# Performance work log

Hardware: AMD Instinct MI355X
Metric: run time of the kernel (lower is better)

Reference implementation:

```python
import jax, jax.numpy as jnp
import numpy as np

EPS = 1e-6
T = 10.0
STEPS = 3
BN_EPS = 1e-5

def _normalize(x, axis):
    n = jnp.sqrt(jnp.sum(x * x, axis=axis, keepdims=True))
    return x / jnp.maximum(n, EPS)

def _vq_step(X, D):
    # X: (B, d, n), D: (B, d, r)
    Dn = _normalize(D, 1)
    Xn = _normalize(X, 1)
    cos = jnp.einsum('bdr,bdn->brn', Dn, Xn)          # (B, r, n)
    C = jax.nn.softmax(cos / T, axis=1)               # softmax over r
    XCt = jnp.einsum('bdn,brn->bdr', X, C)            # (B, d, r)
    sums = jnp.maximum(jnp.sum(C, axis=2), EPS)       # (B, r)
    D2 = _normalize(XCt / sums[:, None, :], 1)
    Xbar = jnp.einsum('bdr,brn->bdn', D2, C)
    return D2, C, Xbar

def _ham_vq(X, D0):
    # K-1 steps without gradient tracking, final step with grad through X only
    Xs = jax.lax.stop_gradient(X)
    def body(D, _):
        D, _, _ = _vq_step(Xs, D)
        return D, None
    D, _ = jax.lax.scan(body, _normalize(D0, 1), None, length=STEPS - 1)
    D = jax.lax.stop_gradient(D)
    _, _, Xbar = _vq_step(X, D)
    return Xbar

def _conv1x1(x, w, b=None):
    y = jnp.einsum('oc,bchw->bohw', w, x)
    if b is not None:
        y = y + b[None, :, None, None]
    return y

def _bn(x, gamma, beta, mean, var):
    inv = gamma / jnp.sqrt(var + BN_EPS)
    return x * inv[None, :, None, None] + (beta - mean * inv)[None, :, None, None]


def setup_inputs() -> dict:
    key = jax.random.key(0)
    ks = jax.random.split(key, 16)
    B, Cin, H, W = 8, 512, 64, 64
    d_mid, r = 512, 64
    out_ch = 2 * d_mid  # dual
    sc = 0.02
    inp = {
        'z': jax.random.normal(ks[0], (B, Cin, H, W), jnp.float32),
        'lower_w': jax.random.normal(ks[1], (out_ch, Cin), jnp.float32) * sc,
        'lower_b': jnp.zeros((out_ch,), jnp.float32),
        'Dinit_s': jax.random.uniform(ks[2], (B, d_mid, r), jnp.float32),
        'Dinit_c': jax.random.uniform(ks[3], (B, d_mid, r), jnp.float32),
        'cheese_w': jax.random.normal(ks[4], (out_ch, out_ch), jnp.float32) * sc,
        'ch_gamma': jnp.ones((out_ch,), jnp.float32),
        'ch_beta': jnp.zeros((out_ch,), jnp.float32),
        'ch_mean': jax.random.normal(ks[5], (out_ch,), jnp.float32) * 0.1,
        'ch_var': jax.random.uniform(ks[6], (out_ch,), jnp.float32) + 0.5,
        'upper_w': jax.random.normal(ks[7], (Cin, out_ch), jnp.float32) * sc,
        'upper_b': jnp.zeros((Cin,), jnp.float32),
        'h_gamma': jnp.ones((Cin,), jnp.float32),
        'h_beta': jnp.zeros((Cin,), jnp.float32),
        'h_mean': jax.random.normal(ks[8], (Cin,), jnp.float32) * 0.1,
        'h_var': jax.random.uniform(ks[9], (Cin,), jnp.float32) + 0.5,
        'coef_ham': jnp.array(1.0, jnp.float32),
        'coef_shortcut': jnp.array(1.0, jnp.float32),
    }
    return inp


def reference(z, lower_w, lower_b, Dinit_s, Dinit_c, cheese_w,
              ch_gamma, ch_beta, ch_mean, ch_var, upper_w, upper_b,
              h_gamma, h_beta, h_mean, h_var, coef_ham, coef_shortcut):
    B, Cin, H, W = z.shape
    identity = z
    # lower: conv1x1 + relu
    y = jax.nn.relu(_conv1x1(z, lower_w, lower_b))       # (B, 2*d_mid, H, W)
    d_mid = y.shape[1] // 2
    y1, y2 = y[:, :d_mid], y[:, d_mid:]
    n = H * W
    # spatial ham
    Xs = y1.reshape(B, d_mid, n)
    y1 = _ham_vq(Xs, Dinit_s).reshape(B, d_mid, H, W)
    # channel ham (same (B, d, n) flattening; HamMD requires dim1 == d_mid)
    Xc = y2.reshape(B, d_mid, n)
    y2 = _ham_vq(Xc, Dinit_c).reshape(B, d_mid, H, W)
    y = jnp.concatenate([y1, y2], axis=1)
    # cheese: conv1x1(no bias) + BN + relu
    y = jax.nn.relu(_bn(_conv1x1(y, cheese_w), ch_gamma, ch_beta, ch_mean, ch_var))
    # upper conv1x1 + BN
    h = _bn(_conv1x1(y, upper_w, upper_b), h_gamma, h_beta, h_mean, h_var)
    out = coef_ham * h + coef_shortcut * identity
    return jax.nn.relu(out)
```

## Files before the change

kernel.cpp:

```cpp
#include <hip/hip_runtime.h>
#include <hip/hip_bf16.h>

typedef __bf16 bf16_t;
typedef __bf16 bf16x4 __attribute__((ext_vector_type(4)));
typedef __bf16 bf16x8 __attribute__((ext_vector_type(8)));
typedef float  f32x4  __attribute__((ext_vector_type(4)));

#define HEPS 1e-6f

__device__ __forceinline__ void gload16(const bf16_t* g, bf16_t* l) {
    __builtin_amdgcn_global_load_lds(
        (const __attribute__((address_space(1))) unsigned int*)(g),
        (__attribute__((address_space(3))) unsigned int*)(l),
        16, 0, 0);
}


__global__ void cvt_all_k(const float* __restrict__ wl, bf16_t* __restrict__ dwl,
                          const float* __restrict__ wc, bf16_t* __restrict__ dwc,
                          const float* __restrict__ wu, bf16_t* __restrict__ dwu) {
    int i = blockIdx.x * 256 + threadIdx.x;
    if (i < 524288) dwl[i] = (bf16_t)wl[i];
    else if (i < 1572864) { int k = i - 524288; dwc[k] = (bf16_t)wc[k]; }
    else { int k = i - 1572864; dwu[k] = (bf16_t)wu[k]; }
}

__global__ void prep_k(const float* __restrict__ chg, const float* __restrict__ chb,
                       const float* __restrict__ chm, const float* __restrict__ chv,
                       const float* __restrict__ hg, const float* __restrict__ hb,
                       const float* __restrict__ hm, const float* __restrict__ hv,
                       const float* __restrict__ ub, const float* __restrict__ cham,
                       float* __restrict__ chA, float* __restrict__ chB,
                       float* __restrict__ hA2, float* __restrict__ hB2) {
    int i = blockIdx.x * 256 + threadIdx.x;
    if (i < 1024) {
        float inv = chg[i] * rsqrtf(chv[i] + 1e-5f);
        chA[i] = inv;
        chB[i] = chb[i] - chm[i] * inv;
    }
    if (i < 512) {
        float inv = hg[i] * rsqrtf(hv[i] + 1e-5f);
        float cA = cham[0];
        hA2[i] = cA * inv;
        hB2[i] = cA * (fmaf(ub[i], inv, hb[i]) - hm[i] * inv);
    }
}

__global__ void tz_k(const float* __restrict__ z, bf16_t* __restrict__ Zt,
                     bf16_t* __restrict__ zb) {
    __shared__ bf16_t t[64][68];
    int b = blockIdx.z, kt = blockIdx.y, nt = blockIdx.x;
    const size_t boff = ((size_t)b * 512 + kt * 64) * 4096 + nt * 64;
    const float* src = z + boff;
    bf16_t* zbo = zb + boff;
    int tid = threadIdx.x;
    int kr = tid >> 4;
    int nc = (tid & 15) * 4;
    #pragma unroll
    for (int it = 0; it < 4; ++it) {
        int k = kr + it * 16;
        float4 v = *(const float4*)&src[(size_t)k * 4096 + nc];
        bf16x4 o;
        o[0] = (bf16_t)v.x; o[1] = (bf16_t)v.y; o[2] = (bf16_t)v.z; o[3] = (bf16_t)v.w;
        t[nc + 0][k] = o[0]; t[nc + 1][k] = o[1];
        t[nc + 2][k] = o[2]; t[nc + 3][k] = o[3];
        *(bf16x4*)&zbo[(size_t)k * 4096 + nc] = o;
    }
    __syncthreads();
    bf16_t* dst = Zt + ((size_t)b * 4096 + nt * 64) * 512 + kt * 64;
    int nr = tid >> 4;
    int kc = (tid & 15) * 4;
    #pragma unroll
    for (int it = 0; it < 4; ++it) {
        int n = nr + it * 16;
        bf16x4 o;
        #pragma unroll
        for (int c = 0; c < 4; ++c) o[c] = t[n][kc + c];
        *(bf16x4*)&dst[(size_t)n * 512 + kc] = o;
    }
}

__global__ void dinit_k(const float* __restrict__ Ds, const float* __restrict__ Dc,
                        bf16_t* __restrict__ Dt) {
    int bs = blockIdx.y;
    int b = bs >> 1;
    const float* src = ((bs & 1) ? Dc : Ds) + (size_t)b * 512 * 64;
    int idx = blockIdx.x * 256 + threadIdx.x;
    int r = idx & 63, d = idx >> 6;
    Dt[(size_t)bs * 64 * 512 + (size_t)r * 512 + d] = (bf16_t)src[d * 64 + r];
}

__global__ void dnorm_k(const bf16_t* __restrict__ Dt, float* __restrict__ dinv) {
    int gw = (blockIdx.x * 256 + threadIdx.x) >> 6;
    int lane = threadIdx.x & 63;
    bf16x8 v = *(const bf16x8*)(Dt + (size_t)gw * 512 + lane * 8);
    float s = 0.f;
    #pragma unroll
    for (int e = 0; e < 8; ++e) { float f = (float)v[e]; s += f * f; }
    #pragma unroll
    for (int off = 32; off > 0; off >>= 1) s += __shfl_xor(s, off);
    if (lane == 0) dinv[gw] = 1.0f / fmaxf(sqrtf(s), HEPS);
}

__global__ void reduce_k(const float* __restrict__ P, bf16_t* __restrict__ Dt,
                         float* __restrict__ dinv) {
    int bsr = blockIdx.x;
    int bs = bsr >> 6, r = bsr & 63;
    int lane = threadIdx.x;
    const float* base = P + ((size_t)(bs * 8) * 64 + r) * 512 + lane * 8;
    float s[8] = {0.f, 0.f, 0.f, 0.f, 0.f, 0.f, 0.f, 0.f};
    #pragma unroll
    for (int kc = 0; kc < 8; ++kc) {
        const float* p = base + (size_t)kc * 64 * 512;
        float4 u = *(const float4*)p;
        float4 w = *(const float4*)(p + 4);
        s[0] += u.x; s[1] += u.y; s[2] += u.z; s[3] += u.w;
        s[4] += w.x; s[5] += w.y; s[6] += w.z; s[7] += w.w;
    }
    bf16x8 o;
    float sq = 0.f;
    #pragma unroll
    for (int e = 0; e < 8; ++e) { sq += s[e] * s[e]; o[e] = (bf16_t)s[e]; }
    *(bf16x8*)&Dt[(size_t)bsr * 512 + lane * 8] = o;
    #pragma unroll
    for (int off = 32; off > 0; off >>= 1) sq += __shfl_xor(sq, off);
    if (lane == 0) dinv[bsr] = 1.0f / fmaxf(sqrtf(sq), HEPS);
}

template<int BM, int BN, int WAVES_M, int WAVES_N, int EPI, int ORDER>
__launch_bounds__(256)
__global__ void g2(const bf16_t* __restrict__ Ag, const bf16_t* __restrict__ Bg,
                   void* __restrict__ Cg, void* __restrict__ C2g,
                   const int M, const int N, const int K,
                   const int ldA, const int ldB, const int ldC,
                   const long aStride, const long bStride,
                   const long cStride, const long c2Stride,
                   const float* __restrict__ p0, const float* __restrict__ p1,
                   const float* __restrict__ scal,
                   const void* __restrict__ shortcut, const long sStride)
{
    constexpr int WM = BM / WAVES_M, WN = BN / WAVES_N;
    constexpr int FM = WM / 16, FN = WN / 16;
    constexpr int ASEG = BM / 64, BSEG = BN / 64;
    constexpr int LPT = ASEG + BSEG;

    __shared__ __align__(64) bf16_t SH[3 * (BM + BN) * 32];
    __shared__ float dl[64];
    bf16_t* Al = SH;
    bf16_t* Bl = SH + 3 * BM * 32;

    const int tid = threadIdx.x;
    const int wave = tid >> 6, lane = tid & 63;
    const int l15 = lane & 15, q = lane >> 4;
    const int lrow = lane >> 2, lcol = (lane & 3) * 8;

    const int gx = gridDim.x, gy = gridDim.y;
    const int per = gx * gy;
    const int nwg = per * gridDim.z;
    const int g = blockIdx.z * per + blockIdx.y * gx + blockIdx.x;
    const int qq = nwg >> 3, rr = nwg & 7;
    const int xcd = g & 7, jj = g >> 3;
    const int w = (xcd < rr ? xcd * (qq + 1) : rr * (qq + 1) + (xcd - rr) * qq) + jj;
    const int bz = w / per;
    const int rem = w - bz * per;
    int bx, by;
    if constexpr (ORDER == 0) { by = rem / gx; bx = rem - by * gx; }
    else                      { bx = rem / gy; by = rem - bx * gy; }

    int bs = bz, exA = 0, exB = 0;
    if constexpr (EPI == 5) { bs = bz >> 3; exA = exB = (bz & 7) * 512; }
    if constexpr (EPI == 7) { exA = (bz & 1) * 512; }

    const int n0 = bx * BN;
    const int m0 = by * BM;
    const int wm0 = (wave / WAVES_N) * WM;
    const int wn0 = (wave % WAVES_N) * WN;

    const bf16_t* Ab;
    const bf16_t* Bb;
    if constexpr (EPI == 6) {
        Ab = Ag + (size_t)(bz >> 1) * (size_t)aStride + (size_t)(bz & 1) * 512;
        Bb = Bg + (size_t)bz * (size_t)bStride;
    } else {
        Ab = Ag + (size_t)bs * (size_t)aStride + exA;
        Bb = Bg + (size_t)bs * (size_t)bStride + exB;
    }

    if constexpr (EPI == 6) { if (tid < 64) dl[tid] = p0[bz * 64 + tid]; }

    auto stage = [&](int buf, int k0) {
        #pragma unroll
        for (int t = 0; t < ASEG; ++t) {
            int seg = wave * ASEG + t;
            gload16(Ab + (size_t)(m0 + seg * 16 + lrow) * ldA + k0 + lcol,
                    &Al[buf * BM * 32 + seg * 512]);
        }
        #pragma unroll
        for (int t = 0; t < BSEG; ++t) {
            int seg = wave * BSEG + t;
            gload16(Bb + (size_t)(n0 + seg * 16 + lrow) * ldB + k0 + lcol,
                    &Bl[buf * BN * 32 + seg * 512]);
        }
    };

    f32x4 acc[FM][FN];
    #pragma unroll
    for (int i = 0; i < FM; ++i)
        #pragma unroll
        for (int j = 0; j < FN; ++j)
            #pragma unroll
            for (int e = 0; e < 4; ++e) acc[i][j][e] = 0.f;

    float xsq[FM];
    #pragma unroll
    for (int i = 0; i < FM; ++i) xsq[i] = 0.f;

    const int nK = K / 32;
    stage(0, 0);
    if (nK > 1) stage(1, 32);

    for (int t = 0; t < nK; ++t) {
        const int cur = t % 3;

        if (t < nK - 1) asm volatile("s_waitcnt vmcnt(%0)" :: "i"(LPT) : "memory");
        else            asm volatile("s_waitcnt vmcnt(0)" ::: "memory");
        asm volatile("s_barrier" ::: "memory");
        __builtin_amdgcn_sched_barrier(0);

        if (t + 2 < nK) stage((t + 2) % 3, (t + 2) * 32);

        bf16x8 af[FM], bfm[FN];
        #pragma unroll
        for (int i = 0; i < FM; ++i)
            af[i] = *(const bf16x8*)&Al[cur * BM * 32 + (wm0 + 16 * i + l15) * 32 + 8 * q];
        #pragma unroll
        for (int j = 0; j < FN; ++j)
            bfm[j] = *(const bf16x8*)&Bl[cur * BN * 32 + (wn0 + 16 * j + l15) * 32 + 8 * q];

        if constexpr (EPI == 6) {
            #pragma unroll
            for (int i = 0; i < FM; ++i)
                #pragma unroll
                for (int e = 0; e < 8; ++e) {
                    float f = (float)af[i][e];
                    xsq[i] = fmaf(f, f, xsq[i]);
                }
        }

        __builtin_amdgcn_s_setprio(1);
        #pragma unroll
        for (int i = 0; i < FM; ++i)
            #pragma unroll
            for (int j = 0; j < FN; ++j)
                acc[i][j] = __builtin_amdgcn_mfma_f32_16x16x32_bf16(af[i], bfm[j], acc[i][j], 0, 0, 0);
        __builtin_amdgcn_s_setprio(0);
    }

    int rowB[FM];
    #pragma unroll
    for (int i = 0; i < FM; ++i) rowB[i] = m0 + wm0 + 16 * i + 4 * q;
    const int colBase = n0 + wn0;

    if constexpr (EPI == 2) {
        bf16_t* O = (bf16_t*)Cg + (size_t)bz * (size_t)cStride;
        #pragma unroll
        for (int j = 0; j < FN; ++j) {
            int col = colBase + 16 * j + l15;
            float a = p0[col], b = p1[col];
            #pragma unroll
            for (int i = 0; i < FM; ++i) {
                int rb = rowB[i];
                #pragma unroll
                for (int e = 0; e < 4; ++e) {
                    float v = fmaxf(fmaf(acc[i][j][e], a, b), 0.f);
                    O[(size_t)(rb + e) * ldC + col] = (bf16_t)v;
                }
            }
        }
    } else if constexpr (EPI == 3) {
        float* O = (float*)Cg + (size_t)bz * (size_t)cStride;
        const bf16_t* scg = (const bf16_t*)shortcut + (size_t)bz * (size_t)sStride;
        bf16_t* SP = SH;
        float cB = scal[0];
        __syncthreads();
        {
            int row = tid >> 1, h = tid & 1;
            #pragma unroll
            for (int u = 0; u < 8; ++u)
                *(bf16x8*)&SP[row * 132 + h * 64 + u * 8] =
                    *(const bf16x8*)&scg[(size_t)(m0 + row) * ldC + n0 + h * 64 + u * 8];
        }
        __syncthreads();
        #pragma unroll
        for (int i = 0; i < FM; ++i) {
            int rl = wm0 + 16 * i + 4 * q;
            #pragma unroll
            for (int e = 0; e < 4; ++e) {
                int row = m0 + rl + e;
                float a = p0[row], b = p1[row];
                #pragma unroll
                for (int j = 0; j < FN; ++j) {
                    int cl = wn0 + 16 * j + l15;
                    float v = fmaf(acc[i][j][e], a, b)
                            + cB * (float)SP[(rl + e) * 132 + cl];
                    O[(size_t)row * ldC + n0 + cl] = fmaxf(v, 0.f);
                }
            }
        }
    } else if constexpr (EPI == 5) {
        float* O = (float*)Cg + (size_t)bz * (size_t)cStride;
        #pragma unroll
        for (int i = 0; i < FM; ++i) {
            int rb = rowB[i];
            #pragma unroll
            for (int j = 0; j < FN; ++j) {
                int col = colBase + 16 * j + l15;
                *(f32x4*)&O[(size_t)col * ldC + rb] = acc[i][j];
            }
        }
    } else if constexpr (EPI == 6) {
        bf16_t* Cc = (bf16_t*)Cg  + (size_t)bz * (size_t)cStride;
        bf16_t* Ct = (bf16_t*)C2g + (size_t)(bz >> 1) * (size_t)c2Stride;
        const int hoff = (bz & 1) * 64;
        const bool doCt = (C2g != nullptr);
        float xs[FM];
        #pragma unroll
        for (int i = 0; i < FM; ++i) {
            float s2 = xsq[i];
            s2 += __shfl_xor(s2, 16);
            s2 += __shfl_xor(s2, 32);
            xs[i] = s2;
        }
        float di[FN];
        #pragma unroll
        for (int j = 0; j < FN; ++j) di[j] = dl[16 * j + l15];
        #pragma unroll
        for (int i = 0; i < FM; ++i) {
            int rb = rowB[i];
            bf16x4 tj[FN];
            #pragma unroll
            for (int e = 0; e < 4; ++e) {
                float s2row = __shfl(xs[i], 4 * q + e);
                float xi = 1.0f / (10.0f * fmaxf(sqrtf(s2row), HEPS));
                float v[FN];
                float mx = -1e30f;
                #pragma unroll
                for (int j = 0; j < FN; ++j) {
                    v[j] = acc[i][j][e] * di[j] * xi;
                    mx = fmaxf(mx, v[j]);
                }
                mx = fmaxf(mx, __shfl_xor(mx, 1));
                mx = fmaxf(mx, __shfl_xor(mx, 2));
                mx = fmaxf(mx, __shfl_xor(mx, 4));
                mx = fmaxf(mx, __shfl_xor(mx, 8));
                float sm = 0.f;
                #pragma unroll
                for (int j = 0; j < FN; ++j) { v[j] = __expf(v[j] - mx); sm += v[j]; }
                sm += __shfl_xor(sm, 1);
                sm += __shfl_xor(sm, 2);
                sm += __shfl_xor(sm, 4);
                sm += __shfl_xor(sm, 8);
                float rs = 1.0f / sm;
                #pragma unroll
                for (int j = 0; j < FN; ++j) {
                    float p = v[j] * rs;
                    tj[j][e] = (bf16_t)p;
                    if (doCt) Ct[(size_t)(rb + e) * 128 + hoff + 16 * j + l15] = (bf16_t)p;
                }
            }
            #pragma unroll
            for (int j = 0; j < FN; ++j)
                *(bf16x4*)&Cc[(size_t)(16 * j + l15) * ldC + rb] = tj[j];
        }
    } else if constexpr (EPI == 7) {
        bf16_t* O = (bf16_t*)Cg + (size_t)(bz >> 1) * (size_t)cStride;
        const int hoff = (bz & 1) * 64;
        #pragma unroll
        for (int j = 0; j < FN; ++j) {
            int col = colBase + 16 * j + l15;
            float di = p0[bz * 64 + col];
            #pragma unroll
            for (int i = 0; i < FM; ++i) {
                int rb = rowB[i];
                #pragma unroll
                for (int e = 0; e < 4; ++e)
                    O[(size_t)(rb + e) * 128 + hoff + col] = (bf16_t)(acc[i][j][e] * di);
            }
        }
    } else if constexpr (EPI == 8) {
        bf16_t* O  = (bf16_t*)Cg  + (size_t)bz * (size_t)cStride;
        bf16_t* O2 = (bf16_t*)C2g + (size_t)bz * (size_t)c2Stride;
        bf16_t* SP = SH;
        __syncthreads();
        #pragma unroll
        for (int j = 0; j < FN; ++j) {
            int cl = wn0 + 16 * j + l15;
            float bias = p0[n0 + cl];
            #pragma unroll
            for (int i = 0; i < FM; ++i) {
                int rl = wm0 + 16 * i + 4 * q;
                #pragma unroll
                for (int e = 0; e < 4; ++e) {
                    float v = fmaxf(acc[i][j][e] + bias, 0.f);
                    bf16_t b = (bf16_t)v;
                    O[(size_t)(m0 + rl + e) * ldC + n0 + cl] = b;
                    SP[cl * 132 + rl + e] = b;
                }
            }
        }
        __syncthreads();
        {
            int dorow = tid >> 1, h = tid & 1;
            #pragma unroll
            for (int u = 0; u < 8; ++u) {
                bf16x8 v = *(const bf16x8*)&SP[dorow * 132 + h * 64 + u * 8];
                *(bf16x8*)&O2[(size_t)(n0 + dorow) * 4096 + m0 + h * 64 + u * 8] = v;
            }
        }
    }
}


extern "C" void kernel_launch(void* const* d_in, const int* in_sizes, int n_in,
                              void* d_out, int out_size, void* d_ws, size_t ws_size,
                              hipStream_t stream) {
    const float* z        = (const float*)d_in[0];
    const float* lower_w  = (const float*)d_in[1];
    const float* lower_b  = (const float*)d_in[2];
    const float* Dinit_s  = (const float*)d_in[3];
    const float* Dinit_c  = (const float*)d_in[4];
    const float* cheese_w = (const float*)d_in[5];
    const float* ch_gamma = (const float*)d_in[6];
    const float* ch_beta  = (const float*)d_in[7];
    const float* ch_mean  = (const float*)d_in[8];
    const float* ch_var   = (const float*)d_in[9];
    const float* upper_w  = (const float*)d_in[10];
    const float* upper_b  = (const float*)d_in[11];
    const float* h_gamma  = (const float*)d_in[12];
    const float* h_beta   = (const float*)d_in[13];
    const float* h_mean   = (const float*)d_in[14];
    const float* h_var    = (const float*)d_in[15];
    const float* coef_ham = (const float*)d_in[16];
    const float* coef_sc  = (const float*)d_in[17];

    char* ws = (char*)d_ws;
    size_t off = 0;
    auto alloc = [&](size_t bytes) -> void* {
        void* p = ws + off;
        off += (bytes + 255) & ~(size_t)255;
        return p;
    };

    bf16_t* Wl   = (bf16_t*)alloc((size_t)1024 * 512 * 2);
    bf16_t* Wc   = (bf16_t*)alloc((size_t)1024 * 1024 * 2);
    bf16_t* Wu   = (bf16_t*)alloc((size_t)512 * 1024 * 2);
    float*  chA  = (float*) alloc(1024 * 4);
    float*  chB  = (float*) alloc(1024 * 4);
    float*  hA2  = (float*) alloc(512 * 4);
    float*  hB2  = (float*) alloc(512 * 4);
    float*  dinv = (float*) alloc(1024 * 4);
    bf16_t* Xbf  = (bf16_t*)alloc((size_t)8 * 1024 * 4096 * 2);
    bf16_t* Xt   = (bf16_t*)alloc((size_t)8 * 4096 * 1024 * 2);
    bf16_t* Zt   = (bf16_t*)alloc((size_t)8 * 4096 * 512 * 2);
    bf16_t* zb   = (bf16_t*)alloc((size_t)8 * 512 * 4096 * 2);
    bf16_t* Cb   = (bf16_t*)alloc((size_t)16 * 64 * 4096 * 2);
    bf16_t* Ct2  = (bf16_t*)alloc((size_t)8 * 4096 * 128 * 2);
    float*  P    = (float*) alloc((size_t)128 * 64 * 512 * 4);
    bf16_t* Dta  = (bf16_t*)alloc((size_t)16 * 64 * 512 * 2);
    bf16_t* Dtb  = (bf16_t*)alloc((size_t)16 * 64 * 512 * 2);
    bf16_t* Eb   = (bf16_t*)alloc((size_t)8 * 1024 * 128 * 2);
    bf16_t* Ycht = Xbf;

    dim3 blk(256);

    cvt_all_k<<<8192, blk, 0, stream>>>(lower_w, Wl, cheese_w, Wc, upper_w, Wu);
    prep_k<<<4, blk, 0, stream>>>(ch_gamma, ch_beta, ch_mean, ch_var,
                                  h_gamma, h_beta, h_mean, h_var,
                                  upper_b, coef_ham, chA, chB, hA2, hB2);
    tz_k<<<dim3(64, 8, 8), blk, 0, stream>>>(z, Zt, zb);
    dinit_k<<<dim3(128, 16), blk, 0, stream>>>(Dinit_s, Dinit_c, Dta);

    g2<128, 128, 2, 2, 8, 0><<<dim3(8, 32, 8), blk, 0, stream>>>(
        Zt, Wl, (void*)Xt, (void*)Xbf, 4096, 1024, 512,
        512, 512, 1024,
        (long)4096 * 512, 0L, (long)4096 * 1024, (long)1024 * 4096,
        lower_b, nullptr, nullptr, nullptr, 0L);

    dnorm_k<<<256, blk, 0, stream>>>(Dta, dinv);

    bf16_t* cur = Dta;
    bf16_t* nxt = Dtb;
    for (int t = 0; t < 3; ++t) {
        g2<128, 64, 4, 1, 6, 0><<<dim3(1, 32, 16), blk, 0, stream>>>(
            Xt, cur, (void*)Cb, (t == 2) ? (void*)Ct2 : nullptr, 4096, 64, 512,
            1024, 512, 4096,
            (long)4096 * 1024, (long)64 * 512, (long)64 * 4096, (long)4096 * 128,
            dinv, nullptr, nullptr, nullptr, 0L);
        g2<64, 64, 2, 2, 5, 0><<<dim3(1, 8, 128), blk, 0, stream>>>(
            Xbf, Cb, (void*)P, nullptr, 512, 64, 512,
            4096, 4096, 512,
            (long)512 * 4096, (long)64 * 4096, (long)64 * 512, 0L,
            nullptr, nullptr, nullptr, nullptr, 0L);
        reduce_k<<<1024, dim3(64), 0, stream>>>(P, nxt, dinv);
        bf16_t* tmp = cur; cur = nxt; nxt = tmp;
    }

    g2<128, 64, 2, 2, 7, 0><<<dim3(1, 8, 16), blk, 0, stream>>>(
        Wc, cur, (void*)Eb, nullptr, 1024, 64, 512,
        1024, 512, 128,
        0L, (long)64 * 512, (long)1024 * 128, 0L,
        dinv, nullptr, nullptr, nullptr, 0L);

    g2<128, 128, 2, 2, 2, 0><<<dim3(8, 32, 8), blk, 0, stream>>>(
        Ct2, Eb, (void*)Ycht, nullptr, 4096, 1024, 128,
        128, 128, 1024,
        (long)4096 * 128, (long)1024 * 128, (long)4096 * 1024, 0L,
        chA, chB, nullptr, nullptr, 0L);

    g2<128, 128, 2, 2, 3, 1><<<dim3(32, 4, 8), blk, 0, stream>>>(
        Wu, Ycht, d_out, nullptr, 512, 4096, 1024,
        1024, 1024, 4096,
        0L, (long)4096 * 1024, (long)512 * 4096, 0L,
        hA2, hB2, coef_sc, zb, (long)512 * 4096);

    (void)in_sizes; (void)n_in; (void)out_size; (void)ws_size;
}
```

Measured before the change: 314.6 us.

## Drop channel-major X copy; compute X·Cᵀ from Xt with in-LDS transpose

```diff
diff --git a/kernel.cpp b/kernel.cpp
--- a/kernel.cpp
+++ b/kernel.cpp
@@ -102,29 +102,114 @@
     if (lane == 0) dinv[gw] = 1.0f / fmaxf(sqrtf(s), HEPS);
 }
 
-__global__ void reduce_k(const float* __restrict__ P, bf16_t* __restrict__ Dt,
-                         float* __restrict__ dinv) {
-    int bsr = blockIdx.x;
-    int bs = bsr >> 6, r = bsr & 63;
-    int lane = threadIdx.x;
-    const float* base = P + ((size_t)(bs * 8) * 64 + r) * 512 + lane * 8;
-    float s[8] = {0.f, 0.f, 0.f, 0.f, 0.f, 0.f, 0.f, 0.f};
-    #pragma unroll
-    for (int kc = 0; kc < 8; ++kc) {
-        const float* p = base + (size_t)kc * 64 * 512;
-        float4 u = *(const float4*)p;
-        float4 w = *(const float4*)(p + 4);
-        s[0] += u.x; s[1] += u.y; s[2] += u.z; s[3] += u.w;
-        s[4] += w.x; s[5] += w.y; s[6] += w.z; s[7] += w.w;
-    }
-    bf16x8 o;
-    float sq = 0.f;
-    #pragma unroll
-    for (int e = 0; e < 8; ++e) { sq += s[e] * s[e]; o[e] = (bf16_t)s[e]; }
-    *(bf16x8*)&Dt[(size_t)bsr * 512 + lane * 8] = o;
-    #pragma unroll
-    for (int off = 32; off > 0; off >>= 1) sq += __shfl_xor(sq, off);
-    if (lane == 0) dinv[bsr] = 1.0f / fmaxf(sqrtf(sq), HEPS);
+__global__ void reduce_k(const float* __restrict__ P, bf16_t* __restrict__ Dt) {
+    int bs = blockIdx.y;
+    int d = blockIdx.x * 4 + (threadIdx.x >> 6);
+    int r = threadIdx.x & 63;
+    float s = 0.f;
+    #pragma unroll
+    for (int kc = 0; kc < 8; ++kc)
+        s += P[(((size_t)(bs * 8 + kc)) * 512 + d) * 64 + r];
+    Dt[((size_t)bs * 64 + r) * 512 + d] = (bf16_t)s;
+}
+
+__launch_bounds__(256)
+__global__ void xct_k(const bf16_t* __restrict__ Cb, const bf16_t* __restrict__ Xt,
+                      float* __restrict__ P) {
+    __shared__ __align__(64) bf16_t Al[3][64 * 32];
+    __shared__ __align__(64) bf16_t Bl[3][64 * 40];
+
+    const int tid = threadIdx.x;
+    const int wave = tid >> 6, lane = tid & 63;
+    const int l15 = lane & 15, q = lane >> 4;
+    const int lrow = lane >> 2, lcol = (lane & 3) * 8;
+
+    const int bz = blockIdx.z;
+    const int bs = bz >> 3, kc = bz & 7;
+    const int b = bs >> 1, s = bs & 1;
+    const int d0 = blockIdx.x * 64;
+
+    const bf16_t* Ab = Cb + (size_t)bs * 64 * 4096 + kc * 512;
+    const bf16_t* Bsrc = Xt + ((size_t)b * 4096 + kc * 512) * 1024 + s * 512 + d0;
+
+    const int bn = tid >> 3;
+    const int dbase = (tid & 7) * 8;
+    const int nswz = bn ^ (((dbase >> 3) & 3) << 3);
+
+    const int wm0 = (wave >> 1) * 32;
+    const int wn0 = (wave & 1) * 32;
+
+    bf16x8 regs[2];
+
+    auto issueB = [&](int t) -> bf16x8 {
+        return *(const bf16x8*)&Bsrc[(size_t)(t * 32 + bn) * 1024 + dbase];
+    };
+    auto issueA = [&](int buf, int t) {
+        gload16(Ab + (size_t)(wave * 16 + lrow) * 4096 + t * 32 + lcol,
+                &Al[buf][wave * 512]);
+    };
+    auto writeB = [&](int buf, bf16x8 v) {
+        #pragma unroll
+        for (int e = 0; e < 8; ++e)
+            Bl[buf][(dbase + e) * 40 + nswz] = v[e];
+    };
+
+    f32x4 acc[2][2];
+    #pragma unroll
+    for (int i = 0; i < 2; ++i)
+        #pragma unroll
+        for (int j = 0; j < 2; ++j)
+            #pragma unroll
+            for (int e = 0; e < 4; ++e) acc[i][j][e] = 0.f;
+
+    const int nK = 16;
+    regs[0] = issueB(0); issueA(0, 0);
+    regs[1] = issueB(1); issueA(1, 1);
+    writeB(0, regs[0]);
+
+    for (int t = 0; t < nK; ++t) {
+        const int cur = t % 3;
+
+        if (t + 1 < nK) asm volatile("s_waitcnt vmcnt(2) lgkmcnt(0)" ::: "memory");
+        else            asm volatile("s_waitcnt vmcnt(0) lgkmcnt(0)" ::: "memory");
+        asm volatile("s_barrier" ::: "memory");
+        __builtin_amdgcn_sched_barrier(0);
+
+        if (t + 2 < nK) {
+            regs[t & 1] = issueB(t + 2);
+            issueA((t + 2) % 3, t + 2);
+        }
+        if (t + 1 < nK) writeB((t + 1) % 3, regs[(t + 1) & 1]);
+
+        bf16x8 af[2], bfm[2];
+        #pragma unroll
+        for (int i = 0; i < 2; ++i)
+            af[i] = *(const bf16x8*)&Al[cur][(wm0 + 16 * i + l15) * 32 + 8 * q];
+        #pragma unroll
+        for (int j = 0; j < 2; ++j) {
+            int d = wn0 + 16 * j + l15;
+            int nq = 8 * (q ^ ((d >> 3) & 3));
+            bfm[j] = *(const bf16x8*)&Bl[cur][d * 40 + nq];
+        }
+        __builtin_amdgcn_s_setprio(1);
+        #pragma unroll
+        for (int i = 0; i < 2; ++i)
+            #pragma unroll
+            for (int j = 0; j < 2; ++j)
+                acc[i][j] = __builtin_amdgcn_mfma_f32_16x16x32_bf16(af[i], bfm[j], acc[i][j], 0, 0, 0);
+        __builtin_amdgcn_s_setprio(0);
+    }
+
+    float* O = P + (size_t)bz * 512 * 64;
+    #pragma unroll
+    for (int i = 0; i < 2; ++i) {
+        int rb = wm0 + 16 * i + 4 * q;
+        #pragma unroll
+        for (int j = 0; j < 2; ++j) {
+            int col = d0 + wn0 + 16 * j + l15;
+            *(f32x4*)&O[(size_t)col * 64 + rb] = acc[i][j];
+        }
+    }
 }
 
 template<int BM, int BN, int WAVES_M, int WAVES_N, int EPI, int ORDER>
@@ -167,8 +252,7 @@
     if constexpr (ORDER == 0) { by = rem / gx; bx = rem - by * gx; }
     else                      { bx = rem / gy; by = rem - bx * gy; }
 
-    int bs = bz, exA = 0, exB = 0;
-    if constexpr (EPI == 5) { bs = bz >> 3; exA = exB = (bz & 7) * 512; }
+    int bs = bz, exA = 0;
     if constexpr (EPI == 7) { exA = (bz & 1) * 512; }
 
     const int n0 = bx * BN;
@@ -183,7 +267,7 @@
         Bb = Bg + (size_t)bz * (size_t)bStride;
     } else {
         Ab = Ag + (size_t)bs * (size_t)aStride + exA;
-        Bb = Bg + (size_t)bs * (size_t)bStride + exB;
+        Bb = Bg + (size_t)bs * (size_t)bStride;
     }
 
     if constexpr (EPI == 6) { if (tid < 64) dl[tid] = p0[bz * 64 + tid]; }
@@ -305,17 +389,6 @@
                             + cB * (float)SP[(rl + e) * 132 + cl];
                     O[(size_t)row * ldC + n0 + cl] = fmaxf(v, 0.f);
                 }
-            }
-        }
-    } else if constexpr (EPI == 5) {
-        float* O = (float*)Cg + (size_t)bz * (size_t)cStride;
-        #pragma unroll
-        for (int i = 0; i < FM; ++i) {
-            int rb = rowB[i];
-            #pragma unroll
-            for (int j = 0; j < FN; ++j) {
-                int col = colBase + 16 * j + l15;
-                *(f32x4*)&O[(size_t)col * ldC + rb] = acc[i][j];
             }
         }
     } else if constexpr (EPI == 6) {
@@ -387,34 +460,19 @@
                     O[(size_t)(rb + e) * 128 + hoff + col] = (bf16_t)(acc[i][j][e] * di);
             }
         }
-    } else if constexpr (EPI == 8) {
-        bf16_t* O  = (bf16_t*)Cg  + (size_t)bz * (size_t)cStride;
-        bf16_t* O2 = (bf16_t*)C2g + (size_t)bz * (size_t)c2Stride;
-        bf16_t* SP = SH;
-        __syncthreads();
+    } else if constexpr (EPI == 9) {
+        bf16_t* O = (bf16_t*)Cg + (size_t)bz * (size_t)cStride;
         #pragma unroll
         for (int j = 0; j < FN; ++j) {
-            int cl = wn0 + 16 * j + l15;
-            float bias = p0[n0 + cl];
+            int col = colBase + 16 * j + l15;
             #pragma unroll
             for (int i = 0; i < FM; ++i) {
-                int rl = wm0 + 16 * i + 4 * q;
-                #pragma unroll
-                for (int e = 0; e < 4; ++e) {
-                    float v = fmaxf(acc[i][j][e] + bias, 0.f);
-                    bf16_t b = (bf16_t)v;
-                    O[(size_t)(m0 + rl + e) * ldC + n0 + cl] = b;
-                    SP[cl * 132 + rl + e] = b;
-                }
-            }
-        }
-        __syncthreads();
-        {
-            int dorow = tid >> 1, h = tid & 1;
-            #pragma unroll
-            for (int u = 0; u < 8; ++u) {
-                bf16x8 v = *(const bf16x8*)&SP[dorow * 132 + h * 64 + u * 8];
-                *(bf16x8*)&O2[(size_t)(n0 + dorow) * 4096 + m0 + h * 64 + u * 8] = v;
+                int rb = rowB[i];
+                bf16x4 t;
+                #pragma unroll
+                for (int e = 0; e < 4; ++e)
+                    t[e] = (bf16_t)fmaxf(acc[i][j][e] + p0[rb + e], 0.f);
+                *(bf16x4*)&O[(size_t)col * ldC + rb] = t;
             }
         }
     }
@@ -459,17 +517,16 @@
     float*  hA2  = (float*) alloc(512 * 4);
     float*  hB2  = (float*) alloc(512 * 4);
     float*  dinv = (float*) alloc(1024 * 4);
-    bf16_t* Xbf  = (bf16_t*)alloc((size_t)8 * 1024 * 4096 * 2);
+    bf16_t* Ycht = (bf16_t*)alloc((size_t)8 * 4096 * 1024 * 2);
     bf16_t* Xt   = (bf16_t*)alloc((size_t)8 * 4096 * 1024 * 2);
     bf16_t* Zt   = (bf16_t*)alloc((size_t)8 * 4096 * 512 * 2);
     bf16_t* zb   = (bf16_t*)alloc((size_t)8 * 512 * 4096 * 2);
     bf16_t* Cb   = (bf16_t*)alloc((size_t)16 * 64 * 4096 * 2);
     bf16_t* Ct2  = (bf16_t*)alloc((size_t)8 * 4096 * 128 * 2);
-    float*  P    = (float*) alloc((size_t)128 * 64 * 512 * 4);
+    float*  P    = (float*) alloc((size_t)128 * 512 * 64 * 4);
     bf16_t* Dta  = (bf16_t*)alloc((size_t)16 * 64 * 512 * 2);
     bf16_t* Dtb  = (bf16_t*)alloc((size_t)16 * 64 * 512 * 2);
     bf16_t* Eb   = (bf16_t*)alloc((size_t)8 * 1024 * 128 * 2);
-    bf16_t* Ycht = Xbf;
 
     dim3 blk(256);
 
@@ -480,10 +537,10 @@
     tz_k<<<dim3(64, 8, 8), blk, 0, stream>>>(z, Zt, zb);
     dinit_k<<<dim3(128, 16), blk, 0, stream>>>(Dinit_s, Dinit_c, Dta);
 
-    g2<128, 128, 2, 2, 8, 0><<<dim3(8, 32, 8), blk, 0, stream>>>(
-        Zt, Wl, (void*)Xt, (void*)Xbf, 4096, 1024, 512,
+    g2<128, 128, 2, 2, 9, 0><<<dim3(32, 8, 8), blk, 0, stream>>>(
+        Wl, Zt, (void*)Xt, nullptr, 1024, 4096, 512,
         512, 512, 1024,
-        (long)4096 * 512, 0L, (long)4096 * 1024, (long)1024 * 4096,
+        0L, (long)4096 * 512, (long)4096 * 1024, 0L,
         lower_b, nullptr, nullptr, nullptr, 0L);
 
     dnorm_k<<<256, blk, 0, stream>>>(Dta, dinv);
@@ -496,12 +553,9 @@
             1024, 512, 4096,
             (long)4096 * 1024, (long)64 * 512, (long)64 * 4096, (long)4096 * 128,
             dinv, nullptr, nullptr, nullptr, 0L);
-        g2<64, 64, 2, 2, 5, 0><<<dim3(1, 8, 128), blk, 0, stream>>>(
-            Xbf, Cb, (void*)P, nullptr, 512, 64, 512,
-            4096, 4096, 512,
-            (long)512 * 4096, (long)64 * 4096, (long)64 * 512, 0L,
-            nullptr, nullptr, nullptr, nullptr, 0L);
-        reduce_k<<<1024, dim3(64), 0, stream>>>(P, nxt, dinv);
+        xct_k<<<dim3(8, 1, 128), blk, 0, stream>>>(Cb, Xt, P);
+        reduce_k<<<dim3(128, 16), blk, 0, stream>>>(P, nxt);
+        dnorm_k<<<256, blk, 0, stream>>>(nxt, dinv);
         bf16_t* tmp = cur; cur = nxt; nxt = tmp;
     }
 
```

Result: slower. 613.6 us (+95.0%).
